# Kernel optimization log

Measured on AMD Instinct MI355X. Metric: run time of the kernel, lower is better.

## Reference

```python
import jax, jax.numpy as jnp
import numpy as np
from jax import lax

DN = ('NCHW', 'OIHW', 'NCHW')

def conv2d(x, k):
    return lax.conv_general_dilated(x, k, (1, 1), 'SAME', dimension_numbers=DN)

def maxpool(x, k):
    # F.max_pool2d pads with -inf (stride 1, odd k -> SAME)
    return lax.reduce_window(x, jnp.array(-jnp.inf, x.dtype), lax.max,
                             (1, 1, k, k), (1, 1, 1, 1), 'SAME')

def avgpool(x, k):
    # F.avg_pool2d default count_include_pad=True -> sum with zero pad / k*k
    s = lax.reduce_window(x, jnp.array(0.0, x.dtype), lax.add,
                          (1, 1, k, k), (1, 1, 1, 1), 'SAME')
    return s / (k * k)

def erode(x, k):
    return -maxpool(-x, k)

def opening(x, k):
    return maxpool(erode(x, k), k)

def quantile(x, q):
    B = x.shape[0]
    return jnp.quantile(x.reshape(B, -1), q, axis=1).reshape(B, 1, 1, 1).astype(x.dtype)

_SOBEL_X = jnp.array([[-1, 0, 1], [-2, 0, 2], [-1, 0, 1]], jnp.float32).reshape(1, 1, 3, 3)
_SOBEL_Y = jnp.array([[1, 2, 1], [0, 0, 0], [-1, -2, -1]], jnp.float32).reshape(1, 1, 3, 3)

def sobelxy(x):
    return jnp.abs(conv2d(x, _SOBEL_X)) + jnp.abs(conv2d(x, _SOBEL_Y))

def _gauss_window(size=11, sigma=1.5):
    g = np.exp(-((np.arange(size) - size // 2) ** 2) / (2.0 * sigma ** 2))
    g = g / g.sum()
    return jnp.asarray(np.outer(g, g), jnp.float32).reshape(1, 1, size, size)

_SSIM_W = _gauss_window()

def ssim(x, y):
    # standard single-channel SSIM, gaussian 11x11 sigma=1.5, SAME padding
    C1, C2 = 0.01 ** 2, 0.03 ** 2
    mu1, mu2 = conv2d(x, _SSIM_W), conv2d(y, _SSIM_W)
    mu1_sq, mu2_sq, mu12 = mu1 * mu1, mu2 * mu2, mu1 * mu2
    s1 = conv2d(x * x, _SSIM_W) - mu1_sq
    s2 = conv2d(y * y, _SSIM_W) - mu2_sq
    s12 = conv2d(x * y, _SSIM_W) - mu12
    m = ((2 * mu12 + C1) * (2 * s12 + C2)) / ((mu1_sq + mu2_sq + C1) * (s1 + s2 + C2))
    return m.mean()

def compute_saliency(ir1):
    # multi-scale morphological top-hat, max over scales, mean-normalized
    sals = [ir1 - opening(ir1, k) for k in (9, 15, 31)]
    sal = jnp.maximum(jnp.maximum(sals[0], sals[1]), sals[2])
    return sal / (sal.mean(axis=(2, 3), keepdims=True) + 1e-6)

def halo_mask_builder(ir1, vis1):
    # surrogate for undefined PhysicsConsistentHaloMask: halo ring around IR highlights
    bright = (ir1 > quantile(ir1, 0.97)).astype(ir1.dtype)
    dilated = maxpool(bright, 15)
    return jnp.clip(dilated - bright, 0.0, 1.0)

_NEAR_RADIUS = 50
_c = np.arange(-_NEAR_RADIUS, _NEAR_RADIUS + 1)
_yy, _xx = np.meshgrid(_c, _c, indexing='ij')
_DISK = jnp.asarray((( _xx * _xx + _yy * _yy) <= _NEAR_RADIUS * _NEAR_RADIUS).astype(np.float32)).reshape(1, 1, 2 * _NEAR_RADIUS + 1, 2 * _NEAR_RADIUS + 1)

def build_distance_decay(M_light):
    near = conv2d((M_light > 0).astype(M_light.dtype), _DISK)
    return (near > 0).astype(M_light.dtype)


def setup_inputs() -> dict:
    key = jax.random.key(0)
    kA, kB, kF = jax.random.split(key, 3)
    shp = (4, 1, 512, 512)
    return {
        'image_A': jax.random.uniform(kA, shp, jnp.float32),
        'image_B': jax.random.uniform(kB, shp, jnp.float32),
        'image_fused': jax.random.uniform(kF, shp, jnp.float32),
    }


def reference(image_A, image_B, image_fused):
    w_l1, w_grad, w_ssim = 15.0, 14.0, 20.0
    lambda_halo, lambda_bloom = 0.3, 0.6
    blur_ks = 9

    ir1 = image_A[:, :1]
    vis1 = image_B[:, :1]
    fused1 = image_fused[:, :1]

    sal = compute_saliency(ir1)
    # get_M_mask: top_ratio_m=0.1, slope=20
    M = jax.nn.sigmoid(20.0 * (sal - quantile(sal, 0.9)))
    # get_M_light_mask
    M_light = ((sal > quantile(sal, 0.97)) & (ir1 > quantile(ir1, 0.97))).astype(sal.dtype)
    M_light = M_light * (vis1 > quantile(vis1, 0.97)).astype(sal.dtype)
    M = lax.stop_gradient(M)
    M_light = lax.stop_gradient(M_light)

    imax = jnp.maximum(image_A, image_B)
    imin = jnp.minimum(image_A, image_B)
    thr_ir = jnp.clip(quantile(image_A, 0.7), 0.45, 0.85)
    thr_vis = jnp.clip(quantile(image_B, 0.4), 0.3, 0.7)
    thr_vis_super = jnp.clip(quantile(image_B, 0.85), 0.75, 0.98)
    ir_bright = image_A > thr_ir
    vis_bright = image_B > thr_vis
    vis_super = image_B > thr_vis_super
    salient = jnp.where(vis_bright, imin, imax)
    salient = jnp.where(vis_super & ir_bright, imax, salient)
    intensity_target = M * salient + (1.0 - M) * imax

    loss_l1 = w_l1 * jnp.abs(image_fused - intensity_target).mean()

    gA, gB, gF = sobelxy(ir1), sobelxy(vis1), sobelxy(fused1)
    loss_grad = w_grad * jnp.abs(gF - jnp.maximum(gA, gB)).mean()

    loss_ssim = w_ssim * (1.0 - (0.5 * ssim(image_A, image_fused)
                                 + 0.5 * ssim(image_B, image_fused)))

    ir_b = avgpool(ir1, blur_ks)
    vis_b = avgpool(vis1, blur_ks)
    fused_b = jnp.clip(avgpool(fused1, blur_ks), 0.0, 1.0)

    halo = halo_mask_builder(ir1, vis1)
    Mhalo = jnp.clip(halo - M_light, 0.0, 1.0) * build_distance_decay(M_light)
    Mhalo = lax.stop_gradient(Mhalo)

    sum_mhalo = jnp.maximum(Mhalo.sum() + 1e-6, 1.0)
    loss_halo = (Mhalo * jax.nn.relu(fused_b - ir_b)).sum() / sum_mhalo
    sum_m = jnp.maximum(M.sum() + 1e-6, 1.0)
    loss_bloom = (M * jax.nn.relu(fused_b - vis_b)).sum() / sum_m

    weighted_hb = lambda_halo * loss_halo + lambda_bloom * loss_bloom
    fusion_loss = loss_l1 + loss_grad + loss_ssim + weighted_hb
    return (fusion_loss, loss_grad, loss_l1, loss_ssim, weighted_hb)
```

## Files before the change

kernel.cpp:

```cpp
#include <hip/hip_runtime.h>
#include <cmath>

#define BATCH 4
#define HGT 512
#define WID 512
#define PIX (HGT*WID)
#define NPIX (BATCH*PIX)

constexpr size_t OFF_SAL   = 0;
constexpr size_t OFF_ML    = OFF_SAL  + (size_t)NPIX*4;
constexpr size_t OFF_HALO  = OFF_ML   + (size_t)NPIX;
constexpr size_t OFF_DECAY = OFF_HALO + (size_t)NPIX;
constexpr size_t OFF_CNT   = OFF_DECAY+ (size_t)NPIX;
constexpr size_t OFF_H1    = OFF_CNT  + 64;
constexpr size_t OFF_H2    = OFF_H1   + (size_t)3*BATCH*4096*4;
constexpr size_t OFF_H3    = OFF_H2   + (size_t)14*BATCH*1024*4;
constexpr size_t OFF_ZEND  = OFF_H3   + (size_t)14*BATCH*1024*4;
constexpr size_t ZERO_BYTES= OFF_ZEND - OFF_DECAY;
constexpr size_t OFF_PTS   = OFF_ZEND;
constexpr size_t OFF_ST1   = OFF_PTS  + (size_t)NPIX*4;
constexpr size_t OFF_ST2   = OFF_ST1  + (size_t)BATCH*16*8;
constexpr size_t OFF_OST   = OFF_ST2  + (size_t)BATCH*16*8;
constexpr size_t OFF_SCAL  = OFF_OST  + (size_t)BATCH*16*4;
constexpr size_t OFF_SPART = OFF_SCAL + (size_t)BATCH*16*4;
constexpr size_t OFF_PG    = OFF_SPART+ 1024*4;
constexpr size_t OFF_PSA   = OFF_PG   + 1024*4;
constexpr size_t OFF_PSB   = OFF_PSA  + 1024*4;
constexpr size_t OFF_P5    = OFF_PSB  + 1024*4;

#define S_THR_IR 0
#define S_THR_VIS 1
#define S_THR_SUP 2
#define S_Q97A 3
#define S_Q97B 4
#define S_Q90S 5
#define S_Q97S 6
#define S_KM 8

#define QH_BLOCKS 128

struct QRanks { int rank[14]; int arr[14]; int nr; };
struct GaussArg { float g[11]; };
struct FracArg { float fA70, fA97, fB40, fB85, fB97, fS90, fS97; };

__device__ __forceinline__ unsigned keymap(float x){
  unsigned u = __float_as_uint(x);
  return (u & 0x80000000u) ? ~u : (u | 0x80000000u);
}
__device__ __forceinline__ float invkey(unsigned k){
  unsigned bits = (k & 0x80000000u) ? (k ^ 0x80000000u) : ~k;
  return __uint_as_float(bits);
}

__device__ __forceinline__ float block_sum(float v, float* red16, int tid){
  for (int o = 32; o > 0; o >>= 1) v += __shfl_down(v, o);
  if ((tid & 63) == 0) red16[tid >> 6] = v;
  __syncthreads();
  float s = (tid < 16) ? red16[tid] : 0.f;
  if (tid < 64) for (int o = 8; o > 0; o >>= 1) s += __shfl_down(s, o);
  __syncthreads();
  return s;
}

__device__ __forceinline__ unsigned block_scan_incl(unsigned own, unsigned* warpsum, int tid){
  unsigned v = own;
  int lane = tid & 63;
  #pragma unroll
  for (int o = 1; o < 64; o <<= 1){
    unsigned t = __shfl_up(v, o, 64);
    if (lane >= o) v += t;
  }
  if (lane == 63) warpsum[tid >> 6] = v;
  __syncthreads();
  if (tid < 16){
    unsigned w = warpsum[tid];
    #pragma unroll
    for (int o = 1; o < 16; o <<= 1){
      unsigned t = __shfl_up(w, o, 64);
      if (tid >= o) w += t;
    }
    warpsum[tid] = w;
  }
  __syncthreads();
  unsigned off = (tid >> 6) ? warpsum[(tid >> 6) - 1] : 0u;
  return v + off;
}

template<int IS_MIN>
__device__ __forceinline__ void sweep31_8(const float* __restrict__ in, int base, int st, float o[8]){
  float a[38];
  #pragma unroll
  for (int j = 0; j < 38; ++j) a[j] = in[base + j*st];
  float core = a[7];
  #pragma unroll
  for (int j = 8; j <= 30; ++j) core = IS_MIN ? fminf(core, a[j]) : fmaxf(core, a[j]);
  float pref[7];
  pref[6] = a[6];
  #pragma unroll
  for (int k = 5; k >= 0; --k) pref[k] = IS_MIN ? fminf(a[k], pref[k+1]) : fmaxf(a[k], pref[k+1]);
  float suf[8];
  suf[1] = a[31];
  #pragma unroll
  for (int k = 2; k <= 7; ++k) suf[k] = IS_MIN ? fminf(suf[k-1], a[30+k]) : fmaxf(suf[k-1], a[30+k]);
  o[0] = IS_MIN ? fminf(pref[0], core) : fmaxf(pref[0], core);
  #pragma unroll
  for (int k = 1; k <= 6; ++k){
    float t = IS_MIN ? fminf(core, suf[k]) : fmaxf(core, suf[k]);
    o[k] = IS_MIN ? fminf(pref[k], t) : fmaxf(pref[k], t);
  }
  o[7] = IS_MIN ? fminf(core, suf[7]) : fmaxf(core, suf[7]);
}

#define RS 97
__global__ __launch_bounds__(1024, 4) void open_k(const float* __restrict__ A,
                                                  float* __restrict__ sal, float* __restrict__ spart){
  __shared__ float buf0[92*RS];
  __shared__ float buf1[92*RS];
  __shared__ float red16[16];
  int b = blockIdx.z;
  int y0 = blockIdx.y*32, x0 = blockIdx.x*32;
  int tid = threadIdx.y*32 + threadIdx.x;
  int ly = threadIdx.y, lx = threadIdx.x;
  const float* Ab = A + ((size_t)b << 18);

  for (int idx = tid; idx < 92*92; idx += 1024){
    int r = idx / 92, c = idx % 92;
    int gy = y0 + r - 30, gx = x0 + c - 30;
    float v = 3.4e38f;
    if (gy >= 0 && gy < HGT && gx >= 0 && gx < WID) v = Ab[(gy << 9) + gx];
    buf0[r*RS + c] = v;
  }
  __syncthreads();
  float centerA = buf0[(ly+30)*RS + lx+30];

  for (int task = tid; task < 92*8; task += 1024){
    int r = task >> 3, seg = task & 7;
    int start = seg*8 - ((seg == 7) ? 2 : 0);
    float o[8];
    sweep31_8<1>(buf0, r*RS + start, 1, o);
    #pragma unroll
    for (int k = 0; k < 8; ++k) buf1[r*RS + start + k] = o[k];
  }
  __syncthreads();
  for (int task = tid; task < 62*8; task += 1024){
    int x = task >> 3, seg = task & 7;
    int start = seg*8 - ((seg == 7) ? 2 : 0);
    float o[8];
    sweep31_8<1>(buf1, start*RS + x, RS, o);
    int gx = x0 + x - 15;
    bool xin = (gx >= 0 && gx < WID);
    #pragma unroll
    for (int k = 0; k < 8; ++k){
      int y = start + k;
      int gy = y0 + y - 15;
      bool in = xin && (gy >= 0) && (gy < HGT);
      buf0[y*RS + x] = in ? o[k] : -3.4e38f;
    }
  }
  __syncthreads();
  for (int task = tid; task < 62*4; task += 1024){
    int r = task >> 2, seg = task & 3;
    int start = seg*8;
    float o[8];
    sweep31_8<0>(buf0, r*RS + start, 1, o);
    #pragma unroll
    for (int k = 0; k < 8; ++k) buf1[r*RS + start + k] = o[k];
  }
  __syncthreads();
  for (int task = tid; task < 32*4; task += 1024){
    int x = task >> 2, seg = task & 3;
    int start = seg*8;
    float o[8];
    sweep31_8<0>(buf1, start*RS + x, RS, o);
    #pragma unroll
    for (int k = 0; k < 8; ++k) buf0[(start+k)*RS + x] = o[k];
  }
  __syncthreads();
  size_t g = ((size_t)b << 18) + ((size_t)(y0+ly) << 9) + (x0+lx);
  float sv = centerA - buf0[ly*RS + lx];
  sal[g] = sv;
  float tot = block_sum(sv, red16, tid);
  if (tid == 0) spart[b*256 + blockIdx.y*16 + blockIdx.x] = tot;
}

__global__ __launch_bounds__(256) void qh1_k(const float* __restrict__ X0, const float* __restrict__ X1,
                                             const float* __restrict__ X2, unsigned* __restrict__ h1){
  __shared__ unsigned hist[4096];
  int b = blockIdx.y, z = blockIdx.z;
  const float* p = (z == 0 ? X0 : (z == 1 ? X1 : X2)) + (size_t)b*PIX;
  const float4* p4 = (const float4*)p;
  for (int i = threadIdx.x; i < 4096; i += 256) hist[i] = 0;
  __syncthreads();
  for (int i = blockIdx.x*256 + threadIdx.x; i < PIX/4; i += QH_BLOCKS*256){
    float4 v = p4[i];
    atomicAdd(&hist[keymap(v.x) >> 20], 1u);
    atomicAdd(&hist[keymap(v.y) >> 20], 1u);
    atomicAdd(&hist[keymap(v.z) >> 20], 1u);
    atomicAdd(&hist[keymap(v.w) >> 20], 1u);
  }
  __syncthreads();
  unsigned* g = h1 + ((size_t)(z*BATCH + b))*4096;
  for (int i = threadIdx.x; i < 4096; i += 256){
    unsigned c = hist[i];
    if (c) atomicAdd(&g[i], c);
  }
}

__global__ __launch_bounds__(1024) void qs1_k(const unsigned* __restrict__ h1, QRanks ra,
                                              int2* __restrict__ st1){
  __shared__ unsigned warpsum[16];
  int zb = blockIdx.x; int z = zb / BATCH, b = zb % BATCH;
  const unsigned* h = h1 + (size_t)zb*4096;
  int t = threadIdx.x, base = t*4;
  unsigned c4[4]; unsigned own = 0;
  for (int j = 0; j < 4; ++j){ c4[j] = h[base+j]; own += c4[j]; }
  unsigned incl = block_scan_incl(own, warpsum, t);
  unsigned excl = incl - own;
  for (int r = 0; r < ra.nr; ++r){
    if (ra.arr[r] != z) continue;
    unsigned rank = (unsigned)ra.rank[r];
    if (rank >= excl && rank < incl){
      unsigned rem = rank - excl;
      for (int j = 0; j < 4; ++j){
        if (rem < c4[j]){ st1[b*16 + r] = make_int2(base + j, (int)rem); break; }
        rem -= c4[j];
      }
    }
  }
}

__global__ __launch_bounds__(256) void qh2_k(const float* __restrict__ X0, const float* __restrict__ X1,
                                             const float* __restrict__ X2,
                                             const int2* __restrict__ st1, QRanks ra,
                                             unsigned* __restrict__ h2){
  __shared__ unsigned hist[6*1024];
  int b = blockIdx.y, z = blockIdx.z;
  int rl[6]; unsigned bins[6]; int nr = 0;
  #pragma unroll
  for (int r = 0; r < 14; ++r){
    if (r < ra.nr && ra.arr[r] == z && nr < 6){
      rl[nr] = r; bins[nr] = (unsigned)st1[b*16 + r].x; ++nr;
    }
  }
  const float* p = (z == 0 ? X0 : (z == 1 ? X1 : X2)) + (size_t)b*PIX;
  const float4* p4 = (const float4*)p;
  for (int i = threadIdx.x; i < 6*1024; i += 256) hist[i] = 0;
  __syncthreads();
  for (int i = blockIdx.x*256 + threadIdx.x; i < PIX/4; i += QH_BLOCKS*256){
    float4 v = p4[i];
    float e[4] = {v.x, v.y, v.z, v.w};
    #pragma unroll
    for (int j = 0; j < 4; ++j){
      unsigned k = keymap(e[j]);
      unsigned top = k >> 20, mid = (k >> 10) & 0x3FFu;
      #pragma unroll
      for (int q = 0; q < 6; ++q)
        if (q < nr && top == bins[q]) atomicAdd(&hist[q*1024 + mid], 1u);
    }
  }
  __syncthreads();
  #pragma unroll
  for (int q = 0; q < 6; ++q){
    if (q >= nr) break;
    unsigned* g = h2 + ((size_t)(rl[q]*BATCH + b))*1024;
    for (int i = threadIdx.x; i < 1024; i += 256){
      unsigned c = hist[q*1024 + i];
      if (c) atomicAdd(&g[i], c);
    }
  }
}

__global__ __launch_bounds__(1024) void qs2_k(const unsigned* __restrict__ h2,
                                              const int2* __restrict__ st1,
                                              int2* __restrict__ st2){
  __shared__ unsigned warpsum[16];
  int rb = blockIdx.x; int r = rb / BATCH, b = rb % BATCH;
  const unsigned* h = h2 + (size_t)rb*1024;
  int t = threadIdx.x;
  unsigned own = h[t];
  unsigned incl = block_scan_incl(own, warpsum, t);
  unsigned excl = incl - own;
  unsigned rank = (unsigned)st1[b*16 + r].y;
  if (rank >= excl && rank < incl) st2[b*16 + r] = make_int2(t, (int)(rank - excl));
}

__global__ __launch_bounds__(256) void qh3_k(const float* __restrict__ X0, const float* __restrict__ X1,
                                             const float* __restrict__ X2,
                                             const int2* __restrict__ st1, const int2* __restrict__ st2,
                                             QRanks ra, unsigned* __restrict__ h3){
  __shared__ unsigned hist[6*1024];
  int b = blockIdx.y, z = blockIdx.z;
  int rl[6]; unsigned key22[6]; int nr = 0;
  #pragma unroll
  for (int r = 0; r < 14; ++r){
    if (r < ra.nr && ra.arr[r] == z && nr < 6){
      rl[nr] = r;
      key22[nr] = (((unsigned)st1[b*16 + r].x) << 10) | (unsigned)st2[b*16 + r].x;
      ++nr;
    }
  }
  const float* p = (z == 0 ? X0 : (z == 1 ? X1 : X2)) + (size_t)b*PIX;
  const float4* p4 = (const float4*)p;
  for (int i = threadIdx.x; i < 6*1024; i += 256) hist[i] = 0;
  __syncthreads();
  for (int i = blockIdx.x*256 + threadIdx.x; i < PIX/4; i += QH_BLOCKS*256){
    float4 v = p4[i];
    float e[4] = {v.x, v.y, v.z, v.w};
    #pragma unroll
    for (int j = 0; j < 4; ++j){
      unsigned k = keymap(e[j]);
      unsigned top22 = k >> 10, low = k & 0x3FFu;
      #pragma unroll
      for (int q = 0; q < 6; ++q)
        if (q < nr && top22 == key22[q]) atomicAdd(&hist[q*1024 + low], 1u);
    }
  }
  __syncthreads();
  #pragma unroll
  for (int q = 0; q < 6; ++q){
    if (q >= nr) break;
    unsigned* g = h3 + ((size_t)(rl[q]*BATCH + b))*1024;
    for (int i = threadIdx.x; i < 1024; i += 256){
      unsigned c = hist[q*1024 + i];
      if (c) atomicAdd(&g[i], c);
    }
  }
}

__global__ __launch_bounds__(1024) void qs3_k(const unsigned* __restrict__ h3,
                                              const int2* __restrict__ st1, const int2* __restrict__ st2,
                                              float* __restrict__ ostat){
  __shared__ unsigned warpsum[16];
  int rb = blockIdx.x; int r = rb / BATCH, b = rb % BATCH;
  const unsigned* h = h3 + (size_t)rb*1024;
  int t = threadIdx.x;
  unsigned own = h[t];
  unsigned incl = block_scan_incl(own, warpsum, t);
  unsigned excl = incl - own;
  unsigned rank = (unsigned)st2[b*16 + r].y;
  if (rank >= excl && rank < incl){
    unsigned key = (((unsigned)st1[b*16 + r].x) << 20) | (((unsigned)st2[b*16 + r].x) << 10) | (unsigned)t;
    ostat[b*16 + r] = invkey(key);
  }
}

__global__ __launch_bounds__(1024) void finq_k(const float* __restrict__ spart,
                                               const float* __restrict__ ostat,
                                               float* __restrict__ scal, FracArg fr){
  __shared__ float red[1024];
  int t = threadIdx.x;
  red[t] = spart[t];
  __syncthreads();
  for (int o = 128; o > 0; o >>= 1){
    if ((t & 255) < o) red[t] += red[t + o];
    __syncthreads();
  }
  if (t < BATCH){
    int b = t;
    const float* o = ostat + b*16;
    float q70  = o[0]  + fr.fA70*(o[1]-o[0]);
    float q97a = o[2]  + fr.fA97*(o[3]-o[2]);
    float q40  = o[4]  + fr.fB40*(o[5]-o[4]);
    float q85  = o[6]  + fr.fB85*(o[7]-o[6]);
    float q97b = o[8]  + fr.fB97*(o[9]-o[8]);
    float q90s = o[10] + fr.fS90*(o[11]-o[10]);
    float q97s = o[12] + fr.fS97*(o[13]-o[12]);
    float c = red[b*256]*(1.0f/(float)PIX) + 1e-6f;
    scal[b*16 + S_THR_IR]  = fminf(fmaxf(q70, 0.45f), 0.85f);
    scal[b*16 + S_Q97A]    = q97a;
    scal[b*16 + S_THR_VIS] = fminf(fmaxf(q40, 0.3f),  0.7f);
    scal[b*16 + S_THR_SUP] = fminf(fmaxf(q85, 0.75f), 0.98f);
    scal[b*16 + S_Q97B]    = q97b;
    scal[b*16 + S_Q90S]    = q90s;
    scal[b*16 + S_Q97S]    = q97s;
    scal[b*16 + S_KM]      = 20.0f / c;
  }
}

__global__ __launch_bounds__(1024) void brighthalo_k(const float* __restrict__ A,
                                                     const float* __restrict__ Bv,
                                                     const float* __restrict__ sal,
                                                     const float* __restrict__ scal,
                                                     unsigned char* __restrict__ halo,
                                                     unsigned char* __restrict__ ml,
                                                     int* __restrict__ cnt, int* __restrict__ pts){
  constexpr int R = 7, TW = 32 + 2*R;
  __shared__ float bt[TW*TW];
  __shared__ float dX[TW*32];
  int b = blockIdx.z;
  float thrA = scal[b*16 + S_Q97A];
  float q97s = scal[b*16 + S_Q97S];
  float q97b = scal[b*16 + S_Q97B];
  int y0 = blockIdx.y*32, x0 = blockIdx.x*32;
  int tid = threadIdx.y*32 + threadIdx.x;
  const float* Ab = A + ((size_t)b << 18);
  for (int idx = tid; idx < TW*TW; idx += 1024){
    int ly = idx / TW, lx = idx % TW;
    int gy = y0 + ly - R, gx = x0 + lx - R;
    float v = 0.f;
    if (gy >= 0 && gy < HGT && gx >= 0 && gx < WID) v = (Ab[(gy << 9) + gx] > thrA) ? 1.f : 0.f;
    bt[idx] = v;
  }
  __syncthreads();
  for (int idx = tid; idx < TW*32; idx += 1024){
    int row = idx >> 5, c = idx & 31;
    float m = 0.f;
    #pragma unroll
    for (int j = 0; j <= 2*R; ++j) m = fmaxf(m, bt[row*TW + c + j]);
    dX[idx] = m;
  }
  __syncthreads();
  int ly = threadIdx.y, lx = threadIdx.x;
  float m = 0.f;
  #pragma unroll
  for (int j = 0; j <= 2*R; ++j) m = fmaxf(m, dX[(ly+j)*32 + lx]);
  bool brightc = bt[(ly+R)*TW + lx + R] > 0.5f;
  size_t g = ((size_t)b << 18) + ((size_t)(y0+ly) << 9) + (x0+lx);
  halo[g] = (m > 0.5f && !brightc) ? 1 : 0;
  bool mlv = brightc && (sal[g] > q97s) && (Bv[g] > q97b);
  ml[g] = mlv ? 1 : 0;
  if (mlv){
    int idx = atomicAdd(&cnt[b], 1);
    pts[((size_t)b << 18) + idx] = (int)(g & (PIX-1));
  }
}

__global__ __launch_bounds__(128) void paint_k(const int* __restrict__ cnt, const int* __restrict__ pts,
                                               unsigned char* __restrict__ decay){
  int b = blockIdx.y;
  int n = cnt[b];
  for (int p = blockIdx.x; p < n; p += gridDim.x){
    int rem = pts[((size_t)b << 18) + p];
    int y = rem >> 9, x = rem & (WID-1);
    int t = threadIdx.x;
    if (t < 101){
      int dy = t - 50;
      int yy = y + dy;
      if (yy >= 0 && yy < HGT){
        int d2 = 2500 - dy*dy;
        int wd = (int)sqrtf((float)d2);
        while ((wd+1)*(wd+1) <= d2) ++wd;
        while (wd*wd > d2) --wd;
        int xl = x - wd; if (xl < 0) xl = 0;
        int xr = x + wd; if (xr > WID-1) xr = WID-1;
        unsigned char* row = decay + ((size_t)b << 18) + (yy << 9);
        int xx = xl;
        while (xx <= xr && (xx & 3)) row[xx++] = 1;
        for (; xx + 3 <= xr; xx += 4) *(unsigned*)(row + xx) = 0x01010101u;
        for (; xx <= xr; ++xx) row[xx] = 1;
      }
    }
  }
}

__device__ __forceinline__ float sobel42(const float* t, int ly, int lx){
  float gx = (t[(ly-1)*42+lx+1] - t[(ly-1)*42+lx-1]) + 2.f*(t[ly*42+lx+1] - t[ly*42+lx-1])
           + (t[(ly+1)*42+lx+1] - t[(ly+1)*42+lx-1]);
  float gy = (t[(ly-1)*42+lx-1] + 2.f*t[(ly-1)*42+lx] + t[(ly-1)*42+lx+1])
           - (t[(ly+1)*42+lx-1] + 2.f*t[(ly+1)*42+lx] + t[(ly+1)*42+lx+1]);
  return fabsf(gx) + fabsf(gy);
}

__global__ __launch_bounds__(1024) void losses_k(const float* __restrict__ A, const float* __restrict__ Bv,
                                                 const float* __restrict__ F, const float* __restrict__ sal,
                                                 const float* __restrict__ scal,
                                                 const unsigned char* __restrict__ ml,
                                                 const unsigned char* __restrict__ halo,
                                                 const unsigned char* __restrict__ decay,
                                                 float* __restrict__ pg,
                                                 float* __restrict__ psa, float* __restrict__ psb,
                                                 float* __restrict__ p5, GaussArg gw){
  __shared__ float smem[12012];
  __shared__ float red16[16];
  int zz = blockIdx.z;
  int y0 = blockIdx.y*32, x0 = blockIdx.x*32;
  int tid = threadIdx.y*32 + threadIdx.x;
  int ly = threadIdx.y, lx = threadIdx.x;

  if (zz < BATCH){
    int b = zz;
    size_t ib = (size_t)b*PIX;
    float* ta = smem; float* tb = smem + 1764; float* tf = smem + 3528;
    float* pl = smem + 5292;
    for (int idx = tid; idx < 42*42; idx += 1024){
      int r = idx/42, c = idx%42;
      int gy = y0 + r - 5, gx = x0 + c - 5;
      float av = 0.f, bv = 0.f, fv = 0.f;
      if (gy >= 0 && gy < HGT && gx >= 0 && gx < WID){
        size_t g = ib + (size_t)gy*WID + gx;
        av = A[g]; bv = Bv[g]; fv = F[g];
      }
      ta[idx] = av; tb[idx] = bv; tf[idx] = fv;
    }
    __syncthreads();
    int blk = (b*gridDim.y + blockIdx.y)*gridDim.x + blockIdx.x;

    float ga = sobel42(ta, ly+5, lx+5), gb = sobel42(tb, ly+5, lx+5), gf = sobel42(tf, ly+5, lx+5);
    float gval = fabsf(gf - fmaxf(ga, gb));
    float gs = block_sum(gval, red16, tid);
    if (tid == 0) pg[blk] = gs;

    float* hx  = pl + 0*1344; float* hxx = pl + 1*1344; float* hxf = pl + 2*1344;
    float* hf  = pl + 3*1344; float* hff = pl + 4*1344;
    for (int idx = tid; idx < 42*32; idx += 1024){
      int row = idx >> 5, col = idx & 31;
      float sf=0.f, sff=0.f;
      for (int j = 0; j < 11; ++j){
        float g = gw.g[j];
        float fv = tf[row*42 + col + j];
        sf += g*fv; sff += g*fv*fv;
      }
      hf[idx]=sf; hff[idx]=sff;
    }
    const float C1 = 1e-4f, C2 = 9e-4f;
    #pragma unroll
    for (int pass = 0; pass < 2; ++pass){
      const float* tx = pass ? tb : ta;
      for (int idx = tid; idx < 42*32; idx += 1024){
        int row = idx >> 5, col = idx & 31;
        float sx=0.f, sxx=0.f, sxf=0.f;
        for (int j = 0; j < 11; ++j){
          float g = gw.g[j];
          float xv = tx[row*42 + col + j], fv = tf[row*42 + col + j];
          sx += g*xv; sxx += g*xv*xv; sxf += g*xv*fv;
        }
        hx[idx]=sx; hxx[idx]=sxx; hxf[idx]=sxf;
      }
      __syncthreads();
      float mu1=0.f, mu2=0.f, cxx=0.f, cff=0.f, cxf=0.f;
      for (int j = 0; j < 11; ++j){
        float g = gw.g[j];
        int o = (ly+j)*32 + lx;
        mu1 += g*hx[o]; mu2 += g*hf[o];
        cxx += g*hxx[o]; cff += g*hff[o]; cxf += g*hxf[o];
      }
      float m11 = mu1*mu1, m22 = mu2*mu2, m12 = mu1*mu2;
      float s1 = cxx - m11, s2 = cff - m22, s12 = cxf - m12;
      float m = ((2.f*m12 + C1)*(2.f*s12 + C2)) / ((m11 + m22 + C1)*(s1 + s2 + C2));
      __syncthreads();
      float s = block_sum(m, red16, tid);
      if (tid == 0){ if (pass) psb[blk] = s; else psa[blk] = s; }
    }
  } else {
    int b = zz - BATCH;
    size_t ib = (size_t)b*PIX;
    float* ti = smem; float* tv = smem + 1600; float* tf = smem + 3200;
    float* hi_ = smem + 4800; float* hv_ = smem + 6080; float* hf_ = smem + 7360;
    for (int idx = tid; idx < 40*40; idx += 1024){
      int r = idx/40, c = idx%40;
      int gy = y0 + r - 4, gx = x0 + c - 4;
      float a = 0.f, v = 0.f, f = 0.f;
      if (gy >= 0 && gy < HGT && gx >= 0 && gx < WID){
        size_t g = ib + (size_t)gy*WID + gx;
        a = A[g]; v = Bv[g]; f = F[g];
      }
      ti[idx] = a; tv[idx] = v; tf[idx] = f;
    }
    __syncthreads();
    for (int idx = tid; idx < 40*32; idx += 1024){
      int row = idx >> 5, col = idx & 31;
      float si=0.f, sv=0.f, sf=0.f;
      for (int j = 0; j < 9; ++j){
        int o = row*40 + col + j;
        si += ti[o]; sv += tv[o]; sf += tf[o];
      }
      hi_[idx]=si; hv_[idx]=sv; hf_[idx]=sf;
    }
    __syncthreads();
    float si=0.f, sv=0.f, sf=0.f;
    for (int j = 0; j < 9; ++j){
      int o = (ly+j)*32 + lx;
      si += hi_[o]; sv += hv_[o]; sf += hf_[o];
    }
    const float inv81 = 1.f/81.f;
    float ib_ = si*inv81, vb_ = sv*inv81;
    float fb_ = fminf(fmaxf(sf*inv81, 0.f), 1.f);
    size_t g = ib + ((size_t)(y0+ly) << 9) + (x0+lx);
    float q90s = scal[b*16 + S_Q90S], kM = scal[b*16 + S_KM];
    float M = 1.f/(1.f + expf(-kM*(sal[g] - q90s)));
    float mh = (halo[g] && !ml[g] && decay[g]) ? 1.f : 0.f;
    float v1 = mh*fmaxf(fb_ - ib_, 0.f);
    float v3 = M*fmaxf(fb_ - vb_, 0.f);
    float a = ti[(ly+4)*40 + lx+4], v = tv[(ly+4)*40 + lx+4], f = tf[(ly+4)*40 + lx+4];
    float imx = fmaxf(a, v), imn = fminf(a, v);
    bool irb = a > scal[b*16 + S_THR_IR];
    bool visb = v > scal[b*16 + S_THR_VIS];
    bool viss = v > scal[b*16 + S_THR_SUP];
    float salient = visb ? imn : imx;
    if (viss && irb) salient = imx;
    float target = M*salient + (1.f - M)*imx;
    float l1v = fabsf(f - target);

    float vals[5] = {v1, mh, v3, M, l1v};
    int blk = (b*gridDim.y + blockIdx.y)*gridDim.x + blockIdx.x;
    #pragma unroll
    for (int q = 0; q < 5; ++q){
      float s = block_sum(vals[q], red16, tid);
      if (tid == 0) p5[blk*5+q] = s;
    }
  }
}

__global__ __launch_bounds__(1024) void final_k(const float* __restrict__ pg,
                                                const float* __restrict__ psa, const float* __restrict__ psb,
                                                const float* __restrict__ p5, float* __restrict__ out){
  __shared__ float red16[16];
  int t = threadIdx.x;
  float sumG = block_sum(pg[t], red16, t);
  float sA   = block_sum(psa[t], red16, t);
  float sB   = block_sum(psb[t], red16, t);
  float s5[5];
  #pragma unroll
  for (int q = 0; q < 5; ++q) s5[q] = block_sum(p5[t*5+q], red16, t);
  if (t == 0){
    const float inv = 1.f/(float)NPIX;
    float loss_grad = 14.f*sumG*inv;
    float loss_ssim = 20.f*(1.f - 0.5f*sA*inv - 0.5f*sB*inv);
    float lh = s5[0] / fmaxf(s5[1] + 1e-6f, 1.f);
    float lb = s5[2] / fmaxf(s5[3] + 1e-6f, 1.f);
    float whb = 0.3f*lh + 0.6f*lb;
    float loss_l1 = 15.f*s5[4]*inv;
    out[0] = loss_l1 + loss_grad + loss_ssim + whb;
    out[1] = loss_grad;
    out[2] = loss_l1;
    out[3] = loss_ssim;
    out[4] = whb;
  }
}

extern "C" void kernel_launch(void* const* d_in, const int* in_sizes, int n_in,
                              void* d_out, int out_size, void* d_ws, size_t ws_size,
                              hipStream_t stream) {
  const float* A  = (const float*)d_in[0];
  const float* Bv = (const float*)d_in[1];
  const float* F  = (const float*)d_in[2];
  float* out = (float*)d_out;
  char* w = (char*)d_ws;

  float* sal = (float*)(w + OFF_SAL);
  unsigned char* ml    = (unsigned char*)(w + OFF_ML);
  unsigned char* halo  = (unsigned char*)(w + OFF_HALO);
  unsigned char* decay = (unsigned char*)(w + OFF_DECAY);
  int* cnt = (int*)(w + OFF_CNT);
  int* pts = (int*)(w + OFF_PTS);
  unsigned* h1 = (unsigned*)(w + OFF_H1);
  unsigned* h2 = (unsigned*)(w + OFF_H2);
  unsigned* h3 = (unsigned*)(w + OFF_H3);
  int2* st1 = (int2*)(w + OFF_ST1);
  int2* st2 = (int2*)(w + OFF_ST2);
  float* ost  = (float*)(w + OFF_OST);
  float* scal = (float*)(w + OFF_SCAL);
  float* spart= (float*)(w + OFF_SPART);
  float* pg  = (float*)(w + OFF_PG);
  float* psa = (float*)(w + OFF_PSA);
  float* psb = (float*)(w + OFF_PSB);
  float* p5  = (float*)(w + OFF_P5);

  dim3 b256(256);
  dim3 gt(WID/32, HGT/32, BATCH), bt(32, 32);

  auto mkrank = [](double q, int* k0, double* fr){
    double pos = q*(double)(PIX-1);
    double fl = floor(pos);
    *k0 = (int)fl; *fr = pos - fl;
  };
  int kA70, kA97, kB40, kB85, kB97, kS90, kS97;
  double fA70, fA97, fB40, fB85, fB97, fS90, fS97;
  mkrank(0.70, &kA70, &fA70); mkrank(0.97, &kA97, &fA97);
  mkrank(0.40, &kB40, &fB40); mkrank(0.85, &kB85, &fB85); mkrank(0.97, &kB97, &fB97);
  mkrank(0.90, &kS90, &fS90); mkrank(0.97, &kS97, &fS97);

  hipMemsetAsync(w + OFF_DECAY, 0, ZERO_BYTES, stream);

  open_k<<<gt, bt, 0, stream>>>(A, sal, spart);

  QRanks ra{};
  {
    int rr[14] = {kA70, kA70+1, kA97, kA97+1,
                  kB40, kB40+1, kB85, kB85+1, kB97, kB97+1,
                  kS90, kS90+1, kS97, kS97+1};
    int aa[14] = {0,0,0,0, 1,1,1,1,1,1, 2,2,2,2};
    for (int i = 0; i < 14; ++i){ ra.rank[i]=rr[i]; ra.arr[i]=aa[i]; }
    ra.nr = 14;
  }
  qh1_k<<<dim3(QH_BLOCKS, BATCH, 3), b256, 0, stream>>>(A, Bv, sal, h1);
  qs1_k<<<3*BATCH, 1024, 0, stream>>>(h1, ra, st1);
  qh2_k<<<dim3(QH_BLOCKS, BATCH, 3), b256, 0, stream>>>(A, Bv, sal, st1, ra, h2);
  qs2_k<<<14*BATCH, 1024, 0, stream>>>(h2, st1, st2);
  qh3_k<<<dim3(QH_BLOCKS, BATCH, 3), b256, 0, stream>>>(A, Bv, sal, st1, st2, ra, h3);
  qs3_k<<<14*BATCH, 1024, 0, stream>>>(h3, st1, st2, ost);
  FracArg fr{(float)fA70, (float)fA97, (float)fB40, (float)fB85, (float)fB97, (float)fS90, (float)fS97};
  finq_k<<<1, 1024, 0, stream>>>(spart, ost, scal, fr);

  brighthalo_k<<<gt, bt, 0, stream>>>(A, Bv, sal, scal, halo, ml, cnt, pts);
  paint_k<<<dim3(256, BATCH), 128, 0, stream>>>(cnt, pts, decay);

  GaussArg ga{};
  {
    double g[11], s = 0.0;
    for (int i = 0; i < 11; ++i){ double d = (double)(i-5); g[i] = exp(-(d*d)/4.5); s += g[i]; }
    for (int i = 0; i < 11; ++i) ga.g[i] = (float)(g[i]/s);
  }
  losses_k<<<dim3(WID/32, HGT/32, 2*BATCH), bt, 0, stream>>>(A, Bv, F, sal, scal, ml, halo, decay,
                                                             pg, psa, psb, p5, ga);

  final_k<<<1, 1024, 0, stream>>>(pg, psa, psb, p5, out);
}
```

Measured before the change: 143.8 us.

## Register-block separable SSIM and box-blur filters with float4 shared loads

The horizontal Gaussian and box passes now have each thread compute four adjacent outputs from 16- or 12-wide float4 register windows. Tiles are padded to a 44-float row stride so those vector loads stay aligned. The vertical passes have 256 threads each produce four output rows from a shared 14- or 12-row register window instead of one output per thread. The aim is to cut redundant shared-memory reads and loop overhead, at the cost of more registers and fewer active threads per block in those phases.

```diff
diff --git a/kernel.cpp b/kernel.cpp
--- a/kernel.cpp
+++ b/kernel.cpp
@@ -453,12 +453,31 @@
   }
 }
 
-__device__ __forceinline__ float sobel42(const float* t, int ly, int lx){
-  float gx = (t[(ly-1)*42+lx+1] - t[(ly-1)*42+lx-1]) + 2.f*(t[ly*42+lx+1] - t[ly*42+lx-1])
-           + (t[(ly+1)*42+lx+1] - t[(ly+1)*42+lx-1]);
-  float gy = (t[(ly-1)*42+lx-1] + 2.f*t[(ly-1)*42+lx] + t[(ly-1)*42+lx+1])
-           - (t[(ly+1)*42+lx-1] + 2.f*t[(ly+1)*42+lx] + t[(ly+1)*42+lx+1]);
+__device__ __forceinline__ float sobel44(const float* t, int ly, int lx){
+  float gx = (t[(ly-1)*44+lx+1] - t[(ly-1)*44+lx-1]) + 2.f*(t[ly*44+lx+1] - t[ly*44+lx-1])
+           + (t[(ly+1)*44+lx+1] - t[(ly+1)*44+lx-1]);
+  float gy = (t[(ly-1)*44+lx-1] + 2.f*t[(ly-1)*44+lx] + t[(ly-1)*44+lx+1])
+           - (t[(ly+1)*44+lx-1] + 2.f*t[(ly+1)*44+lx] + t[(ly+1)*44+lx+1]);
   return fabsf(gx) + fabsf(gy);
+}
+
+__device__ __forceinline__ void ld16(const float* p, float a[16]){
+  float4 q0 = *(const float4*)(p);
+  float4 q1 = *(const float4*)(p+4);
+  float4 q2 = *(const float4*)(p+8);
+  float4 q3 = *(const float4*)(p+12);
+  a[0]=q0.x; a[1]=q0.y; a[2]=q0.z; a[3]=q0.w;
+  a[4]=q1.x; a[5]=q1.y; a[6]=q1.z; a[7]=q1.w;
+  a[8]=q2.x; a[9]=q2.y; a[10]=q2.z; a[11]=q2.w;
+  a[12]=q3.x; a[13]=q3.y; a[14]=q3.z; a[15]=q3.w;
+}
+__device__ __forceinline__ void ld12(const float* p, float a[12]){
+  float4 q0 = *(const float4*)(p);
+  float4 q1 = *(const float4*)(p+4);
+  float4 q2 = *(const float4*)(p+8);
+  a[0]=q0.x; a[1]=q0.y; a[2]=q0.z; a[3]=q0.w;
+  a[4]=q1.x; a[5]=q1.y; a[6]=q1.z; a[7]=q1.w;
+  a[8]=q2.x; a[9]=q2.y; a[10]=q2.z; a[11]=q2.w;
 }
 
 __global__ __launch_bounds__(1024) void losses_k(const float* __restrict__ A, const float* __restrict__ Bv,
@@ -470,7 +489,7 @@
                                                  float* __restrict__ pg,
                                                  float* __restrict__ psa, float* __restrict__ psb,
                                                  float* __restrict__ p5, GaussArg gw){
-  __shared__ float smem[12012];
+  __shared__ __align__(16) float smem[12264];
   __shared__ float red16[16];
   int zz = blockIdx.z;
   int y0 = blockIdx.y*32, x0 = blockIdx.x*32;
@@ -480,8 +499,9 @@
   if (zz < BATCH){
     int b = zz;
     size_t ib = (size_t)b*PIX;
-    float* ta = smem; float* tb = smem + 1764; float* tf = smem + 3528;
-    float* pl = smem + 5292;
+    float* ta = smem; float* tb = smem + 1848; float* tf = smem + 3696;
+    float* hx  = smem + 5544; float* hxx = smem + 6888; float* hxf = smem + 8232;
+    float* hf  = smem + 9576; float* hff = smem + 10920;
     for (int idx = tid; idx < 42*42; idx += 1024){
       int r = idx/42, c = idx%42;
       int gy = y0 + r - 5, gx = x0 + c - 5;
@@ -490,62 +510,105 @@
         size_t g = ib + (size_t)gy*WID + gx;
         av = A[g]; bv = Bv[g]; fv = F[g];
       }
-      ta[idx] = av; tb[idx] = bv; tf[idx] = fv;
+      int o = r*44 + c;
+      ta[o] = av; tb[o] = bv; tf[o] = fv;
     }
     __syncthreads();
     int blk = (b*gridDim.y + blockIdx.y)*gridDim.x + blockIdx.x;
 
-    float ga = sobel42(ta, ly+5, lx+5), gb = sobel42(tb, ly+5, lx+5), gf = sobel42(tf, ly+5, lx+5);
+    float ga = sobel44(ta, ly+5, lx+5), gb = sobel44(tb, ly+5, lx+5), gf = sobel44(tf, ly+5, lx+5);
     float gval = fabsf(gf - fmaxf(ga, gb));
     float gs = block_sum(gval, red16, tid);
     if (tid == 0) pg[blk] = gs;
 
-    float* hx  = pl + 0*1344; float* hxx = pl + 1*1344; float* hxf = pl + 2*1344;
-    float* hf  = pl + 3*1344; float* hff = pl + 4*1344;
-    for (int idx = tid; idx < 42*32; idx += 1024){
-      int row = idx >> 5, col = idx & 31;
-      float sf=0.f, sff=0.f;
-      for (int j = 0; j < 11; ++j){
-        float g = gw.g[j];
-        float fv = tf[row*42 + col + j];
-        sf += g*fv; sff += g*fv*fv;
-      }
-      hf[idx]=sf; hff[idx]=sff;
+    if (tid < 336){
+      int r = tid >> 3, s = tid & 7;
+      float a[16];
+      ld16(&tf[r*44 + 4*s], a);
+      #pragma unroll
+      for (int k = 0; k < 4; ++k){
+        float sf = 0.f, sff = 0.f;
+        #pragma unroll
+        for (int j = 0; j < 11; ++j){
+          float fv = a[k+j];
+          sf += gw.g[j]*fv; sff += gw.g[j]*fv*fv;
+        }
+        hf[r*32 + 4*s + k] = sf; hff[r*32 + 4*s + k] = sff;
+      }
     }
     const float C1 = 1e-4f, C2 = 9e-4f;
     #pragma unroll
     for (int pass = 0; pass < 2; ++pass){
       const float* tx = pass ? tb : ta;
-      for (int idx = tid; idx < 42*32; idx += 1024){
-        int row = idx >> 5, col = idx & 31;
-        float sx=0.f, sxx=0.f, sxf=0.f;
-        for (int j = 0; j < 11; ++j){
-          float g = gw.g[j];
-          float xv = tx[row*42 + col + j], fv = tf[row*42 + col + j];
-          sx += g*xv; sxx += g*xv*xv; sxf += g*xv*fv;
+      if (tid < 336){
+        int r = tid >> 3, s = tid & 7;
+        float ax[16], af[16];
+        ld16(&tx[r*44 + 4*s], ax);
+        ld16(&tf[r*44 + 4*s], af);
+        #pragma unroll
+        for (int k = 0; k < 4; ++k){
+          float sx = 0.f, sxx = 0.f, sxf = 0.f;
+          #pragma unroll
+          for (int j = 0; j < 11; ++j){
+            float xv = ax[k+j], fv = af[k+j];
+            sx += gw.g[j]*xv; sxx += gw.g[j]*xv*xv; sxf += gw.g[j]*xv*fv;
+          }
+          int o = r*32 + 4*s + k;
+          hx[o] = sx; hxx[o] = sxx; hxf[o] = sxf;
         }
-        hx[idx]=sx; hxx[idx]=sxx; hxf[idx]=sxf;
       }
       __syncthreads();
-      float mu1=0.f, mu2=0.f, cxx=0.f, cff=0.f, cxf=0.f;
-      for (int j = 0; j < 11; ++j){
-        float g = gw.g[j];
-        int o = (ly+j)*32 + lx;
-        mu1 += g*hx[o]; mu2 += g*hf[o];
-        cxx += g*hxx[o]; cff += g*hff[o]; cxf += g*hxf[o];
-      }
-      float m11 = mu1*mu1, m22 = mu2*mu2, m12 = mu1*mu2;
-      float s1 = cxx - m11, s2 = cff - m22, s12 = cxf - m12;
-      float m = ((2.f*m12 + C1)*(2.f*s12 + C2)) / ((m11 + m22 + C1)*(s1 + s2 + C2));
-      __syncthreads();
-      float s = block_sum(m, red16, tid);
+      float macc = 0.f;
+      if (tid < 256){
+        int x = tid & 31, seg = tid >> 5;
+        int rs = seg*4;
+        float mu1[4] = {0,0,0,0}, mu2[4] = {0,0,0,0};
+        float cxx[4] = {0,0,0,0}, cff[4] = {0,0,0,0}, cxf[4] = {0,0,0,0};
+        #pragma unroll
+        for (int j = 0; j < 14; ++j){
+          float v = hx[(rs+j)*32 + x];
+          #pragma unroll
+          for (int k = 0; k < 4; ++k) if (j >= k && j <= k+10) mu1[k] += gw.g[j-k]*v;
+        }
+        #pragma unroll
+        for (int j = 0; j < 14; ++j){
+          float v = hf[(rs+j)*32 + x];
+          #pragma unroll
+          for (int k = 0; k < 4; ++k) if (j >= k && j <= k+10) mu2[k] += gw.g[j-k]*v;
+        }
+        #pragma unroll
+        for (int j = 0; j < 14; ++j){
+          float v = hxx[(rs+j)*32 + x];
+          #pragma unroll
+          for (int k = 0; k < 4; ++k) if (j >= k && j <= k+10) cxx[k] += gw.g[j-k]*v;
+        }
+        #pragma unroll
+        for (int j = 0; j < 14; ++j){
+          float v = hff[(rs+j)*32 + x];
+          #pragma unroll
+          for (int k = 0; k < 4; ++k) if (j >= k && j <= k+10) cff[k] += gw.g[j-k]*v;
+        }
+        #pragma unroll
+        for (int j = 0; j < 14; ++j){
+          float v = hxf[(rs+j)*32 + x];
+          #pragma unroll
+          for (int k = 0; k < 4; ++k) if (j >= k && j <= k+10) cxf[k] += gw.g[j-k]*v;
+        }
+        #pragma unroll
+        for (int k = 0; k < 4; ++k){
+          float m11 = mu1[k]*mu1[k], m22 = mu2[k]*mu2[k], m12 = mu1[k]*mu2[k];
+          float s1 = cxx[k] - m11, s2 = cff[k] - m22, s12 = cxf[k] - m12;
+          macc += ((2.f*m12 + C1)*(2.f*s12 + C2)) / ((m11 + m22 + C1)*(s1 + s2 + C2));
+        }
+      }
+      float s = block_sum(macc, red16, tid);
       if (tid == 0){ if (pass) psb[blk] = s; else psa[blk] = s; }
     }
   } else {
     int b = zz - BATCH;
     size_t ib = (size_t)b*PIX;
-    float* ti = smem; float* tv = smem + 1600; float* tf = smem + 3200;
-    float* hi_ = smem + 4800; float* hv_ = smem + 6080; float* hf_ = smem + 7360;
+    float* ti = smem; float* tv = smem + 1760; float* tfb = smem + 3520;
+    float* hi_ = smem + 5280; float* hv_ = smem + 6560; float* hf_ = smem + 7840;
     for (int idx = tid; idx < 40*40; idx += 1024){
       int r = idx/40, c = idx%40;
       int gy = y0 + r - 4, gx = x0 + c - 4;
@@ -554,44 +617,61 @@
         size_t g = ib + (size_t)gy*WID + gx;
         a = A[g]; v = Bv[g]; f = F[g];
       }
-      ti[idx] = a; tv[idx] = v; tf[idx] = f;
+      int o = r*44 + c;
+      ti[o] = a; tv[o] = v; tfb[o] = f;
     }
     __syncthreads();
-    for (int idx = tid; idx < 40*32; idx += 1024){
-      int row = idx >> 5, col = idx & 31;
-      float si=0.f, sv=0.f, sf=0.f;
-      for (int j = 0; j < 9; ++j){
-        int o = row*40 + col + j;
-        si += ti[o]; sv += tv[o]; sf += tf[o];
-      }
-      hi_[idx]=si; hv_[idx]=sv; hf_[idx]=sf;
+    if (tid < 320){
+      int r = tid >> 3, s = tid & 7;
+      float ai[12], av[12], af[12];
+      ld12(&ti[r*44 + 4*s], ai);
+      ld12(&tv[r*44 + 4*s], av);
+      ld12(&tfb[r*44 + 4*s], af);
+      #pragma unroll
+      for (int k = 0; k < 4; ++k){
+        float si = 0.f, sv = 0.f, sf = 0.f;
+        #pragma unroll
+        for (int j = 0; j < 9; ++j){ si += ai[k+j]; sv += av[k+j]; sf += af[k+j]; }
+        int o = r*32 + 4*s + k;
+        hi_[o] = si; hv_[o] = sv; hf_[o] = sf;
+      }
     }
     __syncthreads();
-    float si=0.f, sv=0.f, sf=0.f;
-    for (int j = 0; j < 9; ++j){
-      int o = (ly+j)*32 + lx;
-      si += hi_[o]; sv += hv_[o]; sf += hf_[o];
-    }
-    const float inv81 = 1.f/81.f;
-    float ib_ = si*inv81, vb_ = sv*inv81;
-    float fb_ = fminf(fmaxf(sf*inv81, 0.f), 1.f);
-    size_t g = ib + ((size_t)(y0+ly) << 9) + (x0+lx);
-    float q90s = scal[b*16 + S_Q90S], kM = scal[b*16 + S_KM];
-    float M = 1.f/(1.f + expf(-kM*(sal[g] - q90s)));
-    float mh = (halo[g] && !ml[g] && decay[g]) ? 1.f : 0.f;
-    float v1 = mh*fmaxf(fb_ - ib_, 0.f);
-    float v3 = M*fmaxf(fb_ - vb_, 0.f);
-    float a = ti[(ly+4)*40 + lx+4], v = tv[(ly+4)*40 + lx+4], f = tf[(ly+4)*40 + lx+4];
-    float imx = fmaxf(a, v), imn = fminf(a, v);
-    bool irb = a > scal[b*16 + S_THR_IR];
-    bool visb = v > scal[b*16 + S_THR_VIS];
-    bool viss = v > scal[b*16 + S_THR_SUP];
-    float salient = visb ? imn : imx;
-    if (viss && irb) salient = imx;
-    float target = M*salient + (1.f - M)*imx;
-    float l1v = fabsf(f - target);
-
-    float vals[5] = {v1, mh, v3, M, l1v};
+    float vals[5] = {0.f, 0.f, 0.f, 0.f, 0.f};
+    if (tid < 256){
+      int x = tid & 31, seg = tid >> 5;
+      int rs = seg*4;
+      float si[4] = {0,0,0,0}, sv[4] = {0,0,0,0}, sf[4] = {0,0,0,0};
+      #pragma unroll
+      for (int j = 0; j < 12; ++j){
+        float vi = hi_[(rs+j)*32 + x], vv = hv_[(rs+j)*32 + x], vf = hf_[(rs+j)*32 + x];
+        #pragma unroll
+        for (int k = 0; k < 4; ++k) if (j >= k && j <= k+8){ si[k] += vi; sv[k] += vv; sf[k] += vf; }
+      }
+      float q90s = scal[b*16 + S_Q90S], kM = scal[b*16 + S_KM];
+      float thr_ir = scal[b*16 + S_THR_IR], thr_vis = scal[b*16 + S_THR_VIS], thr_sup = scal[b*16 + S_THR_SUP];
+      const float inv81 = 1.f/81.f;
+      #pragma unroll
+      for (int k = 0; k < 4; ++k){
+        int y = rs + k;
+        float ib_ = si[k]*inv81, vb_ = sv[k]*inv81;
+        float fb_ = fminf(fmaxf(sf[k]*inv81, 0.f), 1.f);
+        size_t g = ib + ((size_t)(y0+y) << 9) + (x0+x);
+        float M = 1.f/(1.f + expf(-kM*(sal[g] - q90s)));
+        float mh = (halo[g] && !ml[g] && decay[g]) ? 1.f : 0.f;
+        vals[0] += mh*fmaxf(fb_ - ib_, 0.f);
+        vals[1] += mh;
+        vals[2] += M*fmaxf(fb_ - vb_, 0.f);
+        vals[3] += M;
+        int co = (y+4)*44 + x + 4;
+        float a = ti[co], v = tv[co], f = tfb[co];
+        float imx = fmaxf(a, v), imn = fminf(a, v);
+        float salient = (v > thr_vis) ? imn : imx;
+        if ((v > thr_sup) && (a > thr_ir)) salient = imx;
+        float target = M*salient + (1.f - M)*imx;
+        vals[4] += fabsf(f - target);
+      }
+    }
     int blk = (b*gridDim.y + blockIdx.y)*gridDim.x + blockIdx.x;
     #pragma unroll
     for (int q = 0; q < 5; ++q){
```

After: 173.6 us. 1.21x slower.
